# Optimization experiments

Measured on AMD Instinct MI355X. Metric: run time of the kernel, lower is better.

Reference implementation:

```python
import jax, jax.numpy as jnp
import numpy as np
from jax import lax

B, H, W, N = 4, 256, 256, 200000
DN = ('NHWC', 'HWIO', 'NHWC')


def _conv(x, w, padding):
    return lax.conv_general_dilated(x, w, (1, 1), padding, dimension_numbers=DN)


def _convT(x, w):
    # ConvTranspose2d(k=3, stride=2, padding=0): out = 2*H + 1
    return lax.conv_transpose(x, w, (2, 2), 'VALID', dimension_numbers=DN)


def setup_inputs() -> dict:
    key = jax.random.key(0)
    ks = jax.random.split(key, 12)
    features = jax.random.normal(ks[0], (N, 32), jnp.float32)
    bi = jax.random.randint(ks[1], (N, 1), 0, B)
    yi = jax.random.randint(ks[2], (N, 1), 0, H)
    xi = jax.random.randint(ks[3], (N, 1), 0, W)
    coors = jnp.concatenate([bi, yi, xi], axis=1).astype(jnp.int32)

    def p(k, shape):
        return jax.random.normal(k, shape, jnp.float32) * 0.05

    return dict(
        features=features, coors=coors, batch_size=B,
        w1=p(ks[4], (3, 3, 32, 64)), b1=p(ks[5], (64,)),
        w2=p(ks[6], (3, 3, 64, 64)), b2=p(ks[7], (64,)),
        w3=p(ks[8], (3, 3, 64, 64)), b3=p(ks[9], (64,)),
        wt=p(ks[10], (3, 3, 64, 64)), bt=p(ks[11], (64,)),
        w5=p(jax.random.fold_in(key, 99), (3, 3, 64, 64)),
        b5=p(jax.random.fold_in(key, 100), (64,)),
    )


def reference(features, coors, batch_size, w1, b1, w2, b2, w3, b3, wt, bt, w5, b5):
    bidx, yidx, xidx = coors[:, 0], coors[:, 1], coors[:, 2]
    # densify sparse voxels: [B,H,W,32]
    x = jnp.zeros((batch_size, H, W, 32), features.dtype).at[bidx, yidx, xidx].add(features)
    # active-site mask of the input sparse tensor
    mask0 = jnp.zeros((batch_size, H, W, 1), features.dtype).at[bidx, yidx, xidx, 0].set(1.0)
    ones3 = jnp.ones((3, 3, 1, 1), features.dtype)

    # SparseConv2d(32->64, k3, s1, p1): output active set = 3x3 dilation of input sites
    mask1 = (_conv(mask0, ones3, 'SAME') > 0).astype(features.dtype)
    h = jax.nn.relu((_conv(x, w1, 'SAME') + b1) * mask1)
    # two SubMConv2d(64,64,3): output restricted to the same active set
    h = jax.nn.relu((_conv(h, w2, 'SAME') + b2) * mask1)
    h = jax.nn.relu((_conv(h, w3, 'SAME') + b3) * mask1)
    # SparseConvTranspose2d(64,64,3,stride=2): active set = transpose-conv dilation
    mask4 = (_convT(mask1, ones3) > 0).astype(features.dtype)  # [B,2H+1,2W+1,1]
    h = jax.nn.relu((_convT(h, wt) + bt) * mask4)
    # ToDense already done implicitly (h is dense); final Conv2d(64,64,3) VALID + ReLU
    out = jax.nn.relu(_conv(h, w5, 'VALID') + b5)  # [B,2H-1,2W-1,64]
    return out
```

## Files before the change

kernel.cpp:

```cpp
#include <hip/hip_runtime.h>

#define BATCH 4
#define HH 256
#define WW 256
#define HT 513
#define HO 511

typedef __attribute__((ext_vector_type(8))) short bf16x8;
typedef __attribute__((ext_vector_type(4))) float f32x4;

__device__ __forceinline__ unsigned short f2bf(float f) {
    unsigned b = __float_as_uint(f);
    unsigned r = (b + 0x7fffu + ((b >> 16) & 1u)) >> 16;
    return (unsigned short)r;
}

typedef __attribute__((address_space(3))) unsigned int lds_u32;
typedef const __attribute__((address_space(1))) unsigned int g_u32;
__device__ __forceinline__ void gload16(const void* g, void* l) {
    __builtin_amdgcn_global_load_lds((g_u32*)g, (lds_u32*)l, 16, 0, 0);
}

__global__ void k_zero(float* __restrict__ p, int n4) {
    int i = blockIdx.x * blockDim.x + threadIdx.x;
    if (i < n4) ((float4*)p)[i] = make_float4(0.f, 0.f, 0.f, 0.f);
}

__global__ void k_scatter(const float* __restrict__ feat,
                          const int* __restrict__ coors,
                          float* __restrict__ x, float* __restrict__ mask0, int N) {
    int t = blockIdx.x * blockDim.x + threadIdx.x;
    int n = t >> 5, c = t & 31;
    if (n >= N) return;
    int b  = coors[n * 3 + 0];
    int y  = coors[n * 3 + 1];
    int xx = coors[n * 3 + 2];
    float f = feat[n * 32 + c];
    int pix = (b * HH + y) * WW + xx;
    atomicAdd(&x[pix * 32 + c], f);
    if (c == 0) mask0[pix] = 1.0f;
}

__global__ void k_mask1(const float* __restrict__ mask0, float* __restrict__ mask1, int total) {
    int t = blockIdx.x * blockDim.x + threadIdx.x;
    if (t >= total) return;
    int xx = t % WW;
    int y  = (t / WW) % HH;
    int b  = t / (WW * HH);
    float m = 0.f;
    #pragma unroll
    for (int dy = -1; dy <= 1; ++dy) {
        int iy = y + dy;
        if ((unsigned)iy >= HH) continue;
        #pragma unroll
        for (int dx = -1; dx <= 1; ++dx) {
            int ix = xx + dx;
            if ((unsigned)ix >= WW) continue;
            m = fmaxf(m, mask0[(b * HH + iy) * WW + ix]);
        }
    }
    mask1[t] = (m > 0.f) ? 1.f : 0.f;
}

__global__ void k_mask4(const float* __restrict__ mask1, float* __restrict__ mask4, int total) {
    int t = blockIdx.x * blockDim.x + threadIdx.x;
    if (t >= total) return;
    int ox = t % HT;
    int oy = (t / HT) % HT;
    int b  = t / (HT * HT);
    float m = 0.f;
    #pragma unroll
    for (int ky = 0; ky < 3; ++ky) {
        int q = oy + ky - 2;
        if ((q & 1) || (unsigned)(q >> 1) >= (unsigned)HH) continue;
        int iy = q >> 1;
        #pragma unroll
        for (int kx = 0; kx < 3; ++kx) {
            int r = ox + kx - 2;
            if ((r & 1) || (unsigned)(r >> 1) >= (unsigned)WW) continue;
            m = fmaxf(m, mask1[(b * HH + iy) * WW + (r >> 1)]);
        }
    }
    mask4[t] = (m > 0.f) ? 1.f : 0.f;
}

__global__ void k_cast(const float* __restrict__ src, unsigned short* __restrict__ dst, int n8) {
    int i = blockIdx.x * blockDim.x + threadIdx.x;
    if (i >= n8) return;
    float4 a = ((const float4*)src)[2 * i];
    float4 c = ((const float4*)src)[2 * i + 1];
    uint4 o;
    o.x = (unsigned)f2bf(a.x) | ((unsigned)f2bf(a.y) << 16);
    o.y = (unsigned)f2bf(a.z) | ((unsigned)f2bf(a.w) << 16);
    o.z = (unsigned)f2bf(c.x) | ((unsigned)f2bf(c.y) << 16);
    o.w = (unsigned)f2bf(c.z) | ((unsigned)f2bf(c.w) << 16);
    ((uint4*)dst)[i] = o;
}

__global__ void k_pack(const float* __restrict__ w, unsigned short* __restrict__ dst, int T) {
    int t = blockIdx.x * blockDim.x + threadIdx.x;
    if (t >= T * 256) return;
    int step = t >> 8;
    int r = t & 255;
    int nb = r >> 6;
    int l = r & 63;
    int k = step * 32 + ((l >> 4) * 8);
    int n = nb * 16 + (l & 15);
    unsigned short tmp[8];
    #pragma unroll
    for (int j = 0; j < 8; ++j) tmp[j] = f2bf(w[(size_t)(k + j) * 64 + n]);
    uint4 o;
    o.x = (unsigned)tmp[0] | ((unsigned)tmp[1] << 16);
    o.y = (unsigned)tmp[2] | ((unsigned)tmp[3] << 16);
    o.z = (unsigned)tmp[4] | ((unsigned)tmp[5] << 16);
    o.w = (unsigned)tmp[6] | ((unsigned)tmp[7] << 16);
    *(uint4*)(dst + (size_t)((step * 4 + nb) * 64 + l) * 8) = o;
}

enum Mode { CONV, CONVT2 };

template <int CIN, int IN_H, int IN_W, int OUT_H, int OUT_W, int PAD,
          Mode MODE, bool MASKED, bool OUT_F32>
__global__ __launch_bounds__(256, 2) void k_conv_mfma(
    const unsigned short* __restrict__ in,
    const unsigned short* __restrict__ bp,
    const float* __restrict__ bias,
    const float* __restrict__ mask,
    const unsigned short* __restrict__ zpg,
    void* __restrict__ outv)
{
    constexpr int H2  = CIN / 32;
    constexpr int XT  = (OUT_W + 255) / 256;
    constexpr int CPX = CIN / 8;
    constexpr int CSH = (CIN == 64) ? 3 : 2;
    constexpr int APX = (MODE == CONV) ? ((CIN == 32) ? 320 : 288) : 160;
    constexpr int NITER = APX * CPX / 256;
    constexpr int BBYTES = 3 * H2 * 4096;

    __shared__ __align__(16) char lds[BBYTES + APX * CIN * 2];

    int nwg  = (int)gridDim.x;
    int orig = (int)blockIdx.x;
    int q8 = nwg >> 3, r8 = nwg & 7;
    int xcd = orig & 7, pos = orig >> 3;
    int blk = (xcd < r8 ? xcd * (q8 + 1) : r8 * (q8 + 1) + (xcd - r8) * q8) + pos;

    int s = blk % XT;
    int y = (blk / XT) % OUT_H;
    int b = blk / (XT * OUT_H);
    int tid  = threadIdx.x;
    int lane = tid & 63;
    int wid  = tid >> 6;
    int m    = lane & 15;
    int quad = lane >> 4;

    int px_base, par;
    if constexpr (MODE == CONV) { px_base = s * 256 + wid * 64; par = 0; }
    else { par = wid & 1; px_base = s * 256 + (wid >> 1) * 128; }

    int nkx, kx0, kxstep;
    if constexpr (MODE == CONV) { nkx = 3; kx0 = 0; kxstep = 1; }
    else { nkx = (par == 0) ? 2 : 1; kx0 = par; kxstep = 2; }

    int t0;
    if constexpr (MODE == CONV) t0 = s * 256 - PAD;
    else                        t0 = s * 128 - 1;

    int pb;
    if constexpr (MODE == CONV) pb = wid * 64 + m;
    else                        pb = (wid >> 1) * 64 + m;

    const unsigned short* lA = (const unsigned short*)(lds + BBYTES);
    const unsigned short* lB = (const unsigned short*)lds;

    f32x4 acc[4][4] = {};

    #pragma unroll
    for (int ky = 0; ky < 3; ++ky) {
        int iy; bool rowv;
        if constexpr (MODE == CONV) {
            iy = y + ky - PAD;
            rowv = (unsigned)iy < (unsigned)IN_H;
        } else {
            int q = y + ky - 2;
            rowv = (!(q & 1)) && ((unsigned)(q >> 1) < (unsigned)IN_H);
            iy = q >> 1;
        }
        if (!rowv) continue;

        const unsigned short* inrow = in + (size_t)(b * IN_H + iy) * IN_W * CIN;

        __syncthreads();

        {
            const uint4* bsrc = (const uint4*)bp + (size_t)ky * 3 * H2 * 256;
            #pragma unroll
            for (int j = 0; j < 3 * H2; ++j)
                gload16(bsrc + j * 256 + tid,
                        lds + (size_t)(j * 256 + (tid & ~63)) * 16);
        }
        #pragma unroll
        for (int j = 0; j < NITER; ++j) {
            int ci = j * 256 + tid;
            int p  = ci >> CSH;
            int cc = ci & (CPX - 1);
            int swz = (CIN == 64) ? (p & 7) : ((p >> 1) & 3);
            int c  = cc ^ swz;
            int t  = t0 + p;
            const unsigned short* g =
                ((unsigned)t < (unsigned)IN_W) ? inrow + (size_t)t * CIN + c * 8 : zpg;
            gload16(g, lds + BBYTES + (size_t)(j * 256 + (tid & ~63)) * 16);
        }
        __syncthreads();

        #pragma unroll
        for (int i = 0; i < 3; ++i) {
            if (i < nkx) {
                int kx = kx0 + i * kxstep;
                int kxo;
                if constexpr (MODE == CONV) kxo = kx;
                else kxo = ((par + kx - 2) >> 1) + 1;
                #pragma unroll
                for (int half = 0; half < H2; ++half) {
                    int tl = kx * H2 + half;
                    const unsigned short* lbt = lB + tl * 2048 + lane * 8;
                    bf16x8 bfr[4];
                    #pragma unroll
                    for (int nb = 0; nb < 4; ++nb)
                        bfr[nb] = *(const bf16x8*)(lbt + nb * 512);
                    #pragma unroll
                    for (int f = 0; f < 4; ++f) {
                        int p = pb + f * 16 + kxo;
                        int swz = (CIN == 64) ? (p & 7) : ((p >> 1) & 3);
                        int c = ((CIN == 64) ? (half * 4 + quad) : quad) ^ swz;
                        bf16x8 a = *(const bf16x8*)(lA + (size_t)p * CIN + c * 8);
                        #pragma unroll
                        for (int nb = 0; nb < 4; ++nb)
                            acc[f][nb] = __builtin_amdgcn_mfma_f32_16x16x32_bf16(
                                a, bfr[nb], acc[f][nb], 0, 0, 0);
                    }
                }
            }
        }
    }

    int n0 = m;
    float bv[4];
    #pragma unroll
    for (int nb = 0; nb < 4; ++nb) bv[nb] = bias[nb * 16 + n0];
    #pragma unroll
    for (int f = 0; f < 4; ++f) {
        #pragma unroll
        for (int reg = 0; reg < 4; ++reg) {
            int i = f * 16 + quad * 4 + reg;
            int pm;
            if constexpr (MODE == CONV) pm = px_base + i;
            else pm = px_base + 2 * i + par;
            if (pm >= OUT_W) continue;
            size_t pix = (size_t)(b * OUT_H + y) * OUT_W + pm;
            float mk = 1.f;
            if constexpr (MASKED) mk = mask[pix];
            #pragma unroll
            for (int nb = 0; nb < 4; ++nb) {
                float o = fmaxf((acc[f][nb][reg] + bv[nb]) * mk, 0.f);
                if constexpr (OUT_F32)
                    ((float*)outv)[pix * 64 + nb * 16 + n0] = o;
                else
                    ((unsigned short*)outv)[pix * 64 + nb * 16 + n0] = f2bf(o);
            }
        }
    }
}

extern "C" void kernel_launch(void* const* d_in, const int* in_sizes, int n_in,
                              void* d_out, int out_size, void* d_ws, size_t ws_size,
                              hipStream_t stream) {
    const float* feat = (const float*)d_in[0];
    const int* coors  = (const int*)d_in[1];
    const float* w1 = (const float*)d_in[3];
    const float* b1 = (const float*)d_in[4];
    const float* w2 = (const float*)d_in[5];
    const float* b2 = (const float*)d_in[6];
    const float* w3 = (const float*)d_in[7];
    const float* b3 = (const float*)d_in[8];
    const float* wt = (const float*)d_in[9];
    const float* bt = (const float*)d_in[10];
    const float* w5 = (const float*)d_in[11];
    const float* b5 = (const float*)d_in[12];

    int N = in_sizes[0] / 32;

    const size_t MB = 1024 * 1024;
    char* ws = (char*)d_ws;
    unsigned short* pk1 = (unsigned short*)(ws);
    unsigned short* pk2 = (unsigned short*)(ws + 36864);
    unsigned short* pk3 = (unsigned short*)(ws + 110592);
    unsigned short* pkt = (unsigned short*)(ws + 184320);
    unsigned short* pk5 = (unsigned short*)(ws + 258048);
    unsigned short* zpg = (unsigned short*)(ws + 960 * 1024);
    float* mask1 = (float*)(ws + 1 * MB);
    float* mask4 = (float*)(ws + 2 * MB);
    float* mask0 = (float*)(ws + 7 * MB);
    float* x_f32 = (float*)(ws + 8 * MB);
    unsigned short* x_bf  = (unsigned short*)(ws + 42 * MB);
    unsigned short* h1    = (unsigned short*)(ws + 59 * MB);
    unsigned short* h2    = (unsigned short*)(ws + 93 * MB);
    unsigned short* h3    = (unsigned short*)(ws + 8 * MB);
    unsigned short* h4    = (unsigned short*)(ws + 42 * MB);

    int nz4 = (262144 + 8388608) / 4;
    k_zero<<<(nz4 + 255) / 256, 256, 0, stream>>>(mask0, nz4);
    k_zero<<<1, 16, 0, stream>>>((float*)zpg, 16);

    k_scatter<<<(N * 32 + 255) / 256, 256, 0, stream>>>(feat, coors, x_f32, mask0, N);

    k_mask1<<<(BATCH * HH * WW) / 256, 256, 0, stream>>>(mask0, mask1, BATCH * HH * WW);
    int m4tot = BATCH * HT * HT;
    k_mask4<<<(m4tot + 255) / 256, 256, 0, stream>>>(mask1, mask4, m4tot);
    k_cast<<<(1048576 + 255) / 256, 256, 0, stream>>>(x_f32, x_bf, 1048576);
    k_pack<<<9, 256, 0, stream>>>(w1, pk1, 9);
    k_pack<<<18, 256, 0, stream>>>(w2, pk2, 18);
    k_pack<<<18, 256, 0, stream>>>(w3, pk3, 18);
    k_pack<<<18, 256, 0, stream>>>(wt, pkt, 18);
    k_pack<<<18, 256, 0, stream>>>(w5, pk5, 18);

    k_conv_mfma<32, 256, 256, 256, 256, 1, CONV, true, false>
        <<<BATCH * HH * 1, 256, 0, stream>>>(x_bf, pk1, b1, mask1, zpg, h1);
    k_conv_mfma<64, 256, 256, 256, 256, 1, CONV, true, false>
        <<<BATCH * HH * 1, 256, 0, stream>>>(h1, pk2, b2, mask1, zpg, h2);
    k_conv_mfma<64, 256, 256, 256, 256, 1, CONV, true, false>
        <<<BATCH * HH * 1, 256, 0, stream>>>(h2, pk3, b3, mask1, zpg, h3);

    k_conv_mfma<64, 256, 256, HT, HT, 0, CONVT2, true, false>
        <<<BATCH * HT * 3, 256, 0, stream>>>(h3, pkt, bt, mask4, zpg, h4);

    k_conv_mfma<64, HT, HT, HO, HO, 0, CONV, false, true>
        <<<BATCH * HO * 2, 256, 0, stream>>>(h4, pk5, b5, nullptr, zpg, (float*)d_out);
}
```

Baseline: 551.2 us.

## Compute two output rows per block sharing staged input rows and weights

Adds a new conv kernel with 512 threads in which two wave groups each compute one of two adjacent output rows. Four input rows and the weights for each ky are staged once in LDS, with ring buffering so the next ky's loads overlap the current ky's compute. Block indices are remapped so consecutive blocks land on the same XCD. This kernel replaces the three stride-1 convs and the final VALID conv; it reduces redundant input-row and weight traffic at the cost of larger LDS use and one block per CU.

```diff
diff --git a/kernel.cpp b/kernel.cpp
--- a/kernel.cpp
+++ b/kernel.cpp
@@ -115,6 +115,151 @@
     o.z = (unsigned)tmp[4] | ((unsigned)tmp[5] << 16);
     o.w = (unsigned)tmp[6] | ((unsigned)tmp[7] << 16);
     *(uint4*)(dst + (size_t)((step * 4 + nb) * 64 + l) * 8) = o;
+}
+
+template <int CIN, int IN_H, int IN_W, int OUT_H, int OUT_W, int PAD,
+          bool MASKED, bool OUT_F32>
+__global__ __launch_bounds__(512, 1) void k_conv2(
+    const unsigned short* __restrict__ in,
+    const unsigned short* __restrict__ bp,
+    const float* __restrict__ bias,
+    const float* __restrict__ mask,
+    const unsigned short* __restrict__ zpg,
+    void* __restrict__ outv)
+{
+    constexpr int H2  = CIN / 32;
+    constexpr int XT  = (OUT_W + 255) / 256;
+    constexpr int CPX = CIN / 8;
+    constexpr int CSH = (CIN == 64) ? 3 : 2;
+    constexpr int APX = (CIN == 32) ? 272 : 264;
+    constexpr int ACH = APX * CPX;
+    constexpr int ASZ = APX * CIN * 2;
+    constexpr int BSZ = 3 * H2 * 4096;
+    constexpr int BCH = 3 * H2 * 256;
+    constexpr int PAIRS = (OUT_H + 1) / 2;
+
+    extern __shared__ __align__(16) char lds[];
+
+    int nwg  = (int)gridDim.x;
+    int orig = (int)blockIdx.x;
+    int q8 = nwg >> 3, r8 = nwg & 7;
+    int xcd = orig & 7, pos = orig >> 3;
+    int blk = (xcd < r8 ? xcd * (q8 + 1) : r8 * (q8 + 1) + (xcd - r8) * q8) + pos;
+
+    int s  = blk % XT;
+    int yp = (blk / XT) % PAIRS;
+    int b  = blk / (XT * PAIRS);
+    int y0 = yp * 2;
+
+    int tid  = threadIdx.x;
+    int lane = tid & 63;
+    int wid  = tid >> 6;
+    int r    = wid >> 2;
+    int ww   = wid & 3;
+    int m    = lane & 15;
+    int quad = lane >> 4;
+
+    int px_base = s * 256 + ww * 64;
+    int pb = ww * 64 + m;
+    int t0 = s * 256 - PAD;
+
+    auto stageA = [&](int rel) {
+        int iy = y0 - PAD + rel;
+        bool rv = (unsigned)iy < (unsigned)IN_H;
+        const unsigned short* inrow = in + (size_t)(b * IN_H + iy) * IN_W * CIN;
+        char* base = lds + 2 * BSZ + (rel % 3) * ASZ;
+        #pragma unroll
+        for (int j = 0; j < (ACH + 511) / 512; ++j) {
+            int ci = j * 512 + tid;
+            if (ci >= ACH) break;
+            int p  = ci >> CSH;
+            int cc = ci & (CPX - 1);
+            int swz = (CIN == 64) ? (p & 7) : ((p >> 1) & 3);
+            int c  = cc ^ swz;
+            int t  = t0 + p;
+            const unsigned short* g = (rv && (unsigned)t < (unsigned)IN_W)
+                ? inrow + (size_t)t * CIN + c * 8 : zpg;
+            gload16(g, base + (size_t)(ci & ~63) * 16);
+        }
+    };
+    auto stageB = [&](int ky) {
+        const uint4* bsrc = (const uint4*)bp + (size_t)ky * BCH;
+        char* base = lds + (ky & 1) * BSZ;
+        #pragma unroll
+        for (int j = 0; j < (BCH + 511) / 512; ++j) {
+            int ci = j * 512 + tid;
+            if (ci >= BCH) break;
+            gload16(bsrc + ci, base + (size_t)(ci & ~63) * 16);
+        }
+    };
+
+    f32x4 acc[4][4] = {};
+
+    auto doKy = [&](int ky) {
+        const unsigned short* lA_ =
+            (const unsigned short*)(lds + 2 * BSZ + ((r + ky) % 3) * ASZ);
+        const unsigned short* lB_ = (const unsigned short*)(lds + (ky & 1) * BSZ);
+        #pragma unroll
+        for (int kx = 0; kx < 3; ++kx) {
+            #pragma unroll
+            for (int half = 0; half < H2; ++half) {
+                int tl = kx * H2 + half;
+                const unsigned short* lbt = lB_ + tl * 2048 + lane * 8;
+                bf16x8 bfr[4];
+                #pragma unroll
+                for (int nb = 0; nb < 4; ++nb)
+                    bfr[nb] = *(const bf16x8*)(lbt + nb * 512);
+                #pragma unroll
+                for (int f = 0; f < 4; ++f) {
+                    int p = pb + f * 16 + kx;
+                    int swz = (CIN == 64) ? (p & 7) : ((p >> 1) & 3);
+                    int c = ((CIN == 64) ? (half * 4 + quad) : quad) ^ swz;
+                    bf16x8 a = *(const bf16x8*)(lA_ + (size_t)p * CIN + c * 8);
+                    #pragma unroll
+                    for (int nb = 0; nb < 4; ++nb)
+                        acc[f][nb] = __builtin_amdgcn_mfma_f32_16x16x32_bf16(
+                            a, bfr[nb], acc[f][nb], 0, 0, 0);
+                }
+            }
+        }
+    };
+
+    stageA(0); stageA(1); stageA(2); stageB(0); stageB(1);
+    __syncthreads();
+    doKy(0);
+    __syncthreads();
+    stageA(3); stageB(2);
+    doKy(1);
+    __syncthreads();
+    doKy(2);
+
+    int y = y0 + r;
+    if (y < OUT_H) {
+        int n0 = m;
+        float bv[4];
+        #pragma unroll
+        for (int nb = 0; nb < 4; ++nb) bv[nb] = bias[nb * 16 + n0];
+        #pragma unroll
+        for (int f = 0; f < 4; ++f) {
+            #pragma unroll
+            for (int reg = 0; reg < 4; ++reg) {
+                int i = f * 16 + quad * 4 + reg;
+                int pm = px_base + i;
+                if (pm >= OUT_W) continue;
+                size_t pix = (size_t)(b * OUT_H + y) * OUT_W + pm;
+                float mk = 1.f;
+                if constexpr (MASKED) mk = mask[pix];
+                #pragma unroll
+                for (int nb = 0; nb < 4; ++nb) {
+                    float o = fmaxf((acc[f][nb][reg] + bv[nb]) * mk, 0.f);
+                    if constexpr (OUT_F32)
+                        ((float*)outv)[pix * 64 + nb * 16 + n0] = o;
+                    else
+                        ((unsigned short*)outv)[pix * 64 + nb * 16 + n0] = f2bf(o);
+                }
+            }
+        }
+    }
 }
 
 enum Mode { CONV, CONVT2 };
@@ -191,7 +336,6 @@
         const unsigned short* inrow = in + (size_t)(b * IN_H + iy) * IN_W * CIN;
 
         __syncthreads();
-
         {
             const uint4* bsrc = (const uint4*)bp + (size_t)ky * 3 * H2 * 256;
             #pragma unroll
@@ -324,16 +468,19 @@
     k_pack<<<18, 256, 0, stream>>>(wt, pkt, 18);
     k_pack<<<18, 256, 0, stream>>>(w5, pk5, 18);
 
-    k_conv_mfma<32, 256, 256, 256, 256, 1, CONV, true, false>
-        <<<BATCH * HH * 1, 256, 0, stream>>>(x_bf, pk1, b1, mask1, zpg, h1);
-    k_conv_mfma<64, 256, 256, 256, 256, 1, CONV, true, false>
-        <<<BATCH * HH * 1, 256, 0, stream>>>(h1, pk2, b2, mask1, zpg, h2);
-    k_conv_mfma<64, 256, 256, 256, 256, 1, CONV, true, false>
-        <<<BATCH * HH * 1, 256, 0, stream>>>(h2, pk3, b3, mask1, zpg, h3);
+    constexpr size_t LDS32 = 2 * 12288 + 3 * (272 * 32 * 2);
+    constexpr size_t LDS64 = 2 * 24576 + 3 * (264 * 64 * 2);
+
+    k_conv2<32, 256, 256, 256, 256, 1, true, false>
+        <<<BATCH * 128 * 1, 512, LDS32, stream>>>(x_bf, pk1, b1, mask1, zpg, h1);
+    k_conv2<64, 256, 256, 256, 256, 1, true, false>
+        <<<BATCH * 128 * 1, 512, LDS64, stream>>>(h1, pk2, b2, mask1, zpg, h2);
+    k_conv2<64, 256, 256, 256, 256, 1, true, false>
+        <<<BATCH * 128 * 1, 512, LDS64, stream>>>(h2, pk3, b3, mask1, zpg, h3);
 
     k_conv_mfma<64, 256, 256, HT, HT, 0, CONVT2, true, false>
         <<<BATCH * HT * 3, 256, 0, stream>>>(h3, pkt, bt, mask4, zpg, h4);
 
-    k_conv_mfma<64, HT, HT, HO, HO, 0, CONV, false, true>
-        <<<BATCH * HO * 2, 256, 0, stream>>>(h4, pk5, b5, nullptr, zpg, (float*)d_out);
-}
+    k_conv2<64, HT, HT, HO, HO, 0, false, true>
+        <<<BATCH * 256 * 2, 512, LDS64, stream>>>(h4, pk5, b5, nullptr, zpg, (float*)d_out);
+}
```

Result: no change. 555.0 us (+0.7%).
